# Optimization experiments

Measured on AMD Instinct MI355X. Metric: run time of the kernel, lower is better.

Reference implementation:

```python
import jax, jax.numpy as jnp
import numpy as np

N = 20000      # nodes
E = 640000     # edges (before self loops)
IN = 256       # in_channels == out_channels (forced by classifier size 4*in)
H1, C1 = 8, 16   # conv1: heads=8, out=16 -> concat 128
H2, C2 = 1, 256  # conv2: heads=1, out=out_channels
B = 4096       # article pairs
NEG_SLOPE = 0.2  # PyG GATv2Conv default negative_slope


def setup_inputs() -> dict:
    key = jax.random.key(0)
    ks = jax.random.split(key, 24)
    s = 0.05
    inp = {
        "gnn_x": jax.random.normal(ks[0], (N, IN), jnp.float32),
        "vanilla_x": jax.random.normal(ks[1], (N, IN), jnp.float32),
        "edge_src": jax.random.randint(ks[2], (E,), 0, N, jnp.int32),
        "edge_dst": jax.random.randint(ks[3], (E,), 0, N, jnp.int32),
        "a1_idx": jax.random.randint(ks[4], (B,), 0, N, jnp.int64),
        "a2_idx": jax.random.randint(ks[5], (B,), 0, N, jnp.int64),
        # conv1 params (lin_l, lin_r, att, bias)
        "Wl1": jax.random.normal(ks[6], (IN, H1 * C1), jnp.float32) * s,
        "bl1": jnp.zeros((H1 * C1,), jnp.float32),
        "Wr1": jax.random.normal(ks[7], (IN, H1 * C1), jnp.float32) * s,
        "br1": jnp.zeros((H1 * C1,), jnp.float32),
        "att1": jax.random.normal(ks[8], (H1, C1), jnp.float32) * s,
        "bias1": jnp.zeros((H1 * C1,), jnp.float32),
        # conv2 params
        "Wl2": jax.random.normal(ks[9], (H1 * C1, H2 * C2), jnp.float32) * s,
        "bl2": jnp.zeros((H2 * C2,), jnp.float32),
        "Wr2": jax.random.normal(ks[10], (H1 * C1, H2 * C2), jnp.float32) * s,
        "br2": jnp.zeros((H2 * C2,), jnp.float32),
        "att2": jax.random.normal(ks[11], (H2, C2), jnp.float32) * s,
        "bias2": jnp.zeros((H2 * C2,), jnp.float32),
        # classifier
        "Wc": jax.random.normal(ks[12], (4 * IN, 1), jnp.float32) * s,
        "bc": jnp.zeros((1,), jnp.float32),
    }
    return inp


def _gatv2_layer(x, src, dst, Wl, bl, Wr, br, att, bias):
    """GATv2Conv: x_l = lin_l(x)[src], x_r = lin_r(x)[dst];
    e = att . leaky_relu(x_l + x_r); segment softmax over dst; scatter-add x_l*alpha."""
    n = x.shape[0]
    h, c = att.shape
    xl = (x @ Wl + bl).reshape(n, h, c)
    xr = (x @ Wr + br).reshape(n, h, c)
    # per-edge attention logits [E, H]
    e = jnp.einsum('ehc,hc->eh', jax.nn.leaky_relu(xl[src] + xr[dst], NEG_SLOPE), att)
    # segment softmax over destination nodes (self loops guarantee non-empty segments)
    emax = jax.ops.segment_max(e, dst, num_segments=n)
    ex = jnp.exp(e - emax[dst])
    denom = jax.ops.segment_sum(ex, dst, num_segments=n)
    alpha = ex / denom[dst]                      # [E, H]
    out = jax.ops.segment_sum(alpha[:, :, None] * xl[src], dst, num_segments=n)  # [N,H,C]
    return out.reshape(n, h * c) + bias          # concat=True (heads=1 identical)


def reference(gnn_x, vanilla_x, Wl1, bl1, Wr1, br1, att1, bias1,
              Wl2, bl2, Wr2, br2, att2, bias2, Wc, bc,
              edge_src, edge_dst, a1_idx, a2_idx):
    n = gnn_x.shape[0]
    loops = jnp.arange(n, dtype=edge_src.dtype)
    src = jnp.concatenate([edge_src, loops])     # PyG add_self_loops=True
    dst = jnp.concatenate([edge_dst, loops])
    x = _gatv2_layer(gnn_x, src, dst, Wl1, bl1, Wr1, br1, att1, bias1)
    x = jax.nn.relu(x)
    x = _gatv2_layer(x, src, dst, Wl2, bl2, Wr2, br2, att2, bias2)
    combined = jnp.concatenate(
        [vanilla_x[a1_idx], vanilla_x[a2_idx], x[a1_idx], x[a2_idx]], axis=1)  # [B, 4*IN]
    logits = combined @ Wc + bc                  # [B, 1]
    return logits
```

## Files before the change

kernel.cpp:

```cpp
#include <hip/hip_runtime.h>
#include <math.h>

#define N_NODES 20000
#define M_PAD   20032
#define E_EDGES 640000
#define ET (E_EDGES + N_NODES)
#define IN_CH 256
#define D1 128
#define D2 256
#define BPAIRS 4096
#define NEG 0.2f
#define LOG2E 1.4426950408889634f

#define HIST_BLOCKS  ((ET + 255) / 256)
#define MARK_BLOCKS  (2 * BPAIRS / 256)
#define WCONV_BLOCKS 512
#define XCONV_BLOCKS (M_PAD * IN_CH / 4 / 4 / 256)

#if __has_builtin(__builtin_amdgcn_exp2f)
#define EXP2F(x) __builtin_amdgcn_exp2f(x)
#else
#define EXP2F(x) exp2f(x)
#endif

typedef __bf16 bf16x8 __attribute__((ext_vector_type(8)));
typedef float  f32x4  __attribute__((ext_vector_type(4)));
typedef float  f32x2  __attribute__((ext_vector_type(2)));
typedef unsigned short u16x4 __attribute__((ext_vector_type(4)));

__device__ __forceinline__ unsigned short f2b(float f) {
    unsigned int u = __float_as_uint(f);
    unsigned int r = u + 0x7FFFu + ((u >> 16) & 1u);
    return (unsigned short)(r >> 16);
}
__device__ __forceinline__ f32x2 up2(unsigned int u) {
    f32x2 r;
    r.x = __uint_as_float(u << 16);
    r.y = __uint_as_float(u & 0xFFFF0000u);
    return r;
}
__device__ __forceinline__ f32x2 lrelu2(f32x2 s) {
    return __builtin_elementwise_max(s, s * NEG);
}
__device__ __forceinline__ float lrelu(float s) { return fmaxf(s, NEG * s); }

__device__ __forceinline__ void unpack8(uint4 u, float* v) {
    v[0] = __uint_as_float(u.x << 16); v[1] = __uint_as_float(u.x & 0xFFFF0000u);
    v[2] = __uint_as_float(u.y << 16); v[3] = __uint_as_float(u.y & 0xFFFF0000u);
    v[4] = __uint_as_float(u.z << 16); v[5] = __uint_as_float(u.z & 0xFFFF0000u);
    v[6] = __uint_as_float(u.w << 16); v[7] = __uint_as_float(u.w & 0xFFFF0000u);
}


__global__ void prep_kernel(
        const float* __restrict__ gnn_x,
        const float* __restrict__ Wl1, const float* __restrict__ Wr1,
        const float* __restrict__ Wl2, const float* __restrict__ Wr2,
        const int* __restrict__ edge_dst,
        const int* __restrict__ a1_raw, const int* __restrict__ a2_raw,
        unsigned short* __restrict__ xb,
        unsigned short* __restrict__ wt1l, unsigned short* __restrict__ wt1r,
        unsigned short* __restrict__ wt2l, unsigned short* __restrict__ wt2r,
        int* __restrict__ count, int* __restrict__ rank,
        int* __restrict__ mark) {
    int bid = blockIdx.x;
    if (bid < HIST_BLOCKS) {
        int e = bid * 256 + threadIdx.x;
        if (e >= ET) return;
        int dst = (e < E_EDGES) ? edge_dst[e] : (e - E_EDGES);
        rank[e] = atomicAdd(&count[dst], 1);
    } else if (bid < HIST_BLOCKS + MARK_BLOCKS) {
        int idx = (bid - HIST_BLOCKS) * 256 + threadIdx.x;
        __shared__ int stride_s;
        if (threadIdx.x == 0) {
            bool i64 = true;
            for (int i = 1; i < 63; i += 2) i64 = i64 && (a1_raw[i] == 0);
            stride_s = i64 ? 2 : 1;
        }
        __syncthreads();
        int stride = stride_s;
        if (idx < BPAIRS) mark[a1_raw[(long)idx * stride]] = 1;
        else mark[a2_raw[(long)(idx - BPAIRS) * stride]] = 1;
    } else if (bid < HIST_BLOCKS + MARK_BLOCKS + WCONV_BLOCKS) {
        int idx = (bid - HIST_BLOCKS - MARK_BLOCKS) * 256 + threadIdx.x;
        int seg = idx >> 15;
        int r = idx & 32767;
        const float* W;
        unsigned short* Wt;
        int k, n, K;
        if (seg < 2) {
            W = seg ? Wr1 : Wl1; Wt = seg ? wt1r : wt1l;
            k = r >> 7; n = r & 127; K = IN_CH;
        } else {
            W = (seg & 1) ? Wr2 : Wl2; Wt = (seg & 1) ? wt2r : wt2l;
            k = r >> 8; n = r & 255; K = D1;
        }
        Wt[n * K + k] = f2b(W[r]);
    } else {
        int tid = (bid - HIST_BLOCKS - MARK_BLOCKS - WCONV_BLOCKS) * 256
                + threadIdx.x;
        const int NQ = M_PAD * IN_CH / 4;
        int q0 = tid * 4;
#pragma unroll
        for (int j = 0; j < 4; j++) {
            int qi = q0 + j;
            if (qi >= NQ) break;
            int e0 = qi * 4;
            int row = e0 >> 8;
            u16x4 o;
            if (row < N_NODES) {
                f32x4 v = __builtin_nontemporal_load((const f32x4*)(gnn_x + e0));
                o.x = f2b(v.x); o.y = f2b(v.y); o.z = f2b(v.z); o.w = f2b(v.w);
            } else {
                o.x = o.y = o.z = o.w = 0;
            }
            __builtin_nontemporal_store(o, (u16x4*)(xb + e0));
        }
    }
}


__global__ __launch_bounds__(1024) void scan_kernel(const int* __restrict__ count,
                                                    int* __restrict__ offsets) {
    const int PER = 20;
    int t = threadIdx.x;
    int base = t * PER;
    int local[PER];
    int sum = 0;
#pragma unroll
    for (int i = 0; i < PER; i++) {
        int idx = base + i;
        int v = (idx < N_NODES) ? count[idx] : 0;
        local[i] = sum;
        sum += v;
    }
    int lane = t & 63, wave = t >> 6;
    int s = sum;
#pragma unroll
    for (int off = 1; off < 64; off <<= 1) {
        int x = __shfl_up(s, off);
        if (lane >= off) s += x;
    }
    __shared__ int wsum[16];
    __shared__ int wpre[16];
    if (lane == 63) wsum[wave] = s;
    __syncthreads();
    if (t == 0) {
        int acc = 0;
        for (int w = 0; w < 16; w++) { wpre[w] = acc; acc += wsum[w]; }
        offsets[N_NODES] = acc;
    }
    __syncthreads();
    int thread_excl = wpre[wave] + (s - sum);
#pragma unroll
    for (int i = 0; i < PER; i++) {
        int idx = base + i;
        if (idx < N_NODES) offsets[idx] = thread_excl + local[i];
    }
}

__global__ void scatter_kernel(const int* __restrict__ edge_src,
                               const int* __restrict__ edge_dst,
                               const int* __restrict__ rank,
                               const int* __restrict__ offsets,
                               int* __restrict__ sorted_src) {
    int e = blockIdx.x * blockDim.x + threadIdx.x;
    if (e >= ET) return;
    int dst = (e < E_EDGES) ? edge_dst[e] : (e - E_EDGES);
    int src = (e < E_EDGES) ? edge_src[e] : (e - E_EDGES);
    sorted_src[offsets[dst] + rank[e]] = src;
}


template <int K>
__global__ __launch_bounds__(256) void dual_gemm_mfma_kernel(
        const unsigned short* __restrict__ A,
        const unsigned short* __restrict__ Wtl,
        const unsigned short* __restrict__ Wtr,
        const float* __restrict__ bl, const float* __restrict__ br,
        unsigned short* __restrict__ Yl, unsigned short* __restrict__ Yr,
        int M, int NOUT) {
    const int NK = K / 32;
    int wave = threadIdx.x >> 6;
    int lane = threadIdx.x & 63;
    int row0 = blockIdx.x * 64;
    int col0 = (blockIdx.y * 4 + wave) * 16;
    int rsub = lane & 15;
    int koff = (lane >> 4) * 8;

    const unsigned short* ap  = A   + (size_t)(row0 + rsub) * K + koff;
    const unsigned short* bpl = Wtl + (size_t)(col0 + rsub) * K + koff;
    const unsigned short* bpr = Wtr + (size_t)(col0 + rsub) * K + koff;

    bf16x8 bfl[NK], bfr[NK];
#pragma unroll
    for (int kb = 0; kb < NK; kb++) {
        bfl[kb] = *(const bf16x8*)(bpl + kb * 32);
        bfr[kb] = *(const bf16x8*)(bpr + kb * 32);
    }

    f32x4 l0 = {0.f, 0.f, 0.f, 0.f};
    f32x4 l1 = l0, l2 = l0, l3 = l0, r0 = l0, r1 = l0, r2 = l0, r3 = l0;

#pragma unroll
    for (int kb = 0; kb < NK; kb++) {
        int off = kb * 32;
        bf16x8 a0 = *(const bf16x8*)(ap + off);
        bf16x8 a1 = *(const bf16x8*)(ap + 16 * K + off);
        bf16x8 a2 = *(const bf16x8*)(ap + 32 * K + off);
        bf16x8 a3 = *(const bf16x8*)(ap + 48 * K + off);
        l0 = __builtin_amdgcn_mfma_f32_16x16x32_bf16(a0, bfl[kb], l0, 0, 0, 0);
        r0 = __builtin_amdgcn_mfma_f32_16x16x32_bf16(a0, bfr[kb], r0, 0, 0, 0);
        l1 = __builtin_amdgcn_mfma_f32_16x16x32_bf16(a1, bfl[kb], l1, 0, 0, 0);
        r1 = __builtin_amdgcn_mfma_f32_16x16x32_bf16(a1, bfr[kb], r1, 0, 0, 0);
        l2 = __builtin_amdgcn_mfma_f32_16x16x32_bf16(a2, bfl[kb], l2, 0, 0, 0);
        r2 = __builtin_amdgcn_mfma_f32_16x16x32_bf16(a2, bfr[kb], r2, 0, 0, 0);
        l3 = __builtin_amdgcn_mfma_f32_16x16x32_bf16(a3, bfl[kb], l3, 0, 0, 0);
        r3 = __builtin_amdgcn_mfma_f32_16x16x32_bf16(a3, bfr[kb], r3, 0, 0, 0);
    }

    int colg = col0 + rsub;
    float bvl = bl[colg];
    float bvr = br[colg];
    int rbase = row0 + (lane >> 4) * 4;
#pragma unroll
    for (int t = 0; t < 4; t++) {
        f32x4 al = (t == 0) ? l0 : (t == 1) ? l1 : (t == 2) ? l2 : l3;
        f32x4 ar = (t == 0) ? r0 : (t == 1) ? r1 : (t == 2) ? r2 : r3;
#pragma unroll
        for (int r = 0; r < 4; r++) {
            int row = rbase + t * 16 + r;
            if (row < M) {
                Yl[(size_t)row * NOUT + colg] = f2b(al[r] + bvl);
                Yr[(size_t)row * NOUT + colg] = f2b(ar[r] + bvr);
            }
        }
    }
}


__global__ __launch_bounds__(256) void aggregate1_kernel(
        const unsigned short* __restrict__ xl1, const unsigned short* __restrict__ xr1,
        const float* __restrict__ att1, const float* __restrict__ bias1,
        const int* __restrict__ offsets, const int* __restrict__ sorted_src,
        unsigned short* __restrict__ x1) {
    int wave = threadIdx.x >> 6;
    int lane = threadIdx.x & 63;
    int q = lane >> 4;
    int ql = lane & 15;
    int dst = blockIdx.x * 4 + wave;
    if (dst >= M_PAD) return;
    int c0 = ql * 8;
    if (dst >= N_NODES) {
        if (q == 0) {
            uint4 z; z.x = z.y = z.z = z.w = 0;
            *(uint4*)(x1 + (size_t)dst * D1 + c0) = z;
        }
        return;
    }

    uint4 xu = *(const uint4*)(xr1 + (size_t)dst * D1 + c0);
    f32x2 xr[4] = {up2(xu.x), up2(xu.y), up2(xu.z), up2(xu.w)};
    float4 aa0 = *(const float4*)(att1 + c0);
    float4 aa1 = *(const float4*)(att1 + c0 + 4);
    f32x2 att[4];
    att[0].x = aa0.x * LOG2E; att[0].y = aa0.y * LOG2E;
    att[1].x = aa0.z * LOG2E; att[1].y = aa0.w * LOG2E;
    att[2].x = aa1.x * LOG2E; att[2].y = aa1.y * LOG2E;
    att[3].x = aa1.z * LOG2E; att[3].y = aa1.w * LOG2E;

    int beg = offsets[dst], end = offsets[dst + 1];
    const unsigned short* base = xl1 + c0;

    float l = 0.f;
    f32x2 acc[4] = {{0.f,0.f},{0.f,0.f},{0.f,0.f},{0.f,0.f}};

    int i = beg;
    int s0 = sorted_src[min(i + q, end - 1)];
    uint4 g0 = *(const uint4*)(base + (size_t)s0 * D1);
    while (true) {
        int inext = i + 4;
        bool more = inext < end;
        uint4 g1;
        if (more) {
            int s1 = sorted_src[min(inext + q, end - 1)];
            g1 = *(const uint4*)(base + (size_t)s1 * D1);
        }
        bool act = (i + q) < end;
        f32x2 v0 = up2(g0.x), v1 = up2(g0.y), v2 = up2(g0.z), v3 = up2(g0.w);
        f32x2 p2 = att[0] * lrelu2(v0 + xr[0]);
        p2 += att[1] * lrelu2(v1 + xr[1]);
        p2 += att[2] * lrelu2(v2 + xr[2]);
        p2 += att[3] * lrelu2(v3 + xr[3]);
        float p = p2.x + p2.y;
        p += __shfl_xor(p, 1);
        float w = act ? EXP2F(p) : 0.f;
        l += w;
        acc[0] += w * v0; acc[1] += w * v1; acc[2] += w * v2; acc[3] += w * v3;
        if (!more) break;
        i = inext; g0 = g1;
    }
    l += __shfl_xor(l, 16);
    l += __shfl_xor(l, 32);
#pragma unroll
    for (int j = 0; j < 4; j++) {
        f32x2 t;
        t.x = __shfl_xor(acc[j].x, 16); t.y = __shfl_xor(acc[j].y, 16);
        acc[j] += t;
        t.x = __shfl_xor(acc[j].x, 32); t.y = __shfl_xor(acc[j].y, 32);
        acc[j] += t;
    }
    if (q == 0) {
        float inv = 1.f / l;
        float4 bb0 = *(const float4*)(bias1 + c0);
        float4 bb1 = *(const float4*)(bias1 + c0 + 4);
        unsigned short o[8];
        o[0] = f2b(fmaxf(acc[0].x * inv + bb0.x, 0.f));
        o[1] = f2b(fmaxf(acc[0].y * inv + bb0.y, 0.f));
        o[2] = f2b(fmaxf(acc[1].x * inv + bb0.z, 0.f));
        o[3] = f2b(fmaxf(acc[1].y * inv + bb0.w, 0.f));
        o[4] = f2b(fmaxf(acc[2].x * inv + bb1.x, 0.f));
        o[5] = f2b(fmaxf(acc[2].y * inv + bb1.y, 0.f));
        o[6] = f2b(fmaxf(acc[3].x * inv + bb1.z, 0.f));
        o[7] = f2b(fmaxf(acc[3].y * inv + bb1.w, 0.f));
        uint4 ov;
        ov.x = (unsigned int)o[0] | ((unsigned int)o[1] << 16);
        ov.y = (unsigned int)o[2] | ((unsigned int)o[3] << 16);
        ov.z = (unsigned int)o[4] | ((unsigned int)o[5] << 16);
        ov.w = (unsigned int)o[6] | ((unsigned int)o[7] << 16);
        *(uint4*)(x1 + (size_t)dst * D1 + c0) = ov;
    }
}


__global__ __launch_bounds__(256) void aggregate2_kernel(
        const unsigned short* __restrict__ xl2, const unsigned short* __restrict__ xr2,
        const float* __restrict__ att2, const float* __restrict__ bias2,
        const int* __restrict__ offsets, const int* __restrict__ sorted_src,
        const int* __restrict__ mark,
        float* __restrict__ x2) {
    int wave = threadIdx.x >> 6;
    int lane = threadIdx.x & 63;
    int half = lane >> 5;
    int hl = lane & 31;
    int dst = blockIdx.x * 4 + wave;
    if (dst >= N_NODES) return;
    if (!mark[dst]) return;
    int c0 = hl * 8;

    float xr[8], att[8];
    unpack8(*(const uint4*)(xr2 + (size_t)dst * D2 + c0), xr);
#pragma unroll
    for (int j = 0; j < 8; j++) att[j] = att2[c0 + j] * LOG2E;
    int beg = offsets[dst], end = offsets[dst + 1];

    float l = 0.f;
    float acc[8];
#pragma unroll
    for (int j = 0; j < 8; j++) acc[j] = 0.f;

    int i = beg;
    for (; i + 4 <= end; i += 4) {
        int sA = sorted_src[i + half];
        int sB = sorted_src[i + 2 + half];
        float vA[8], vB[8];
        unpack8(*(const uint4*)(xl2 + (size_t)sA * D2 + c0), vA);
        unpack8(*(const uint4*)(xl2 + (size_t)sB * D2 + c0), vB);
        float pA = 0.f, pB = 0.f;
#pragma unroll
        for (int j = 0; j < 8; j++) pA = fmaf(att[j], lrelu(vA[j] + xr[j]), pA);
#pragma unroll
        for (int j = 0; j < 8; j++) pB = fmaf(att[j], lrelu(vB[j] + xr[j]), pB);
        pA += __shfl_xor(pA, 1);  pB += __shfl_xor(pB, 1);
        pA += __shfl_xor(pA, 2);  pB += __shfl_xor(pB, 2);
        pA += __shfl_xor(pA, 4);  pB += __shfl_xor(pB, 4);
        pA += __shfl_xor(pA, 8);  pB += __shfl_xor(pB, 8);
        pA += __shfl_xor(pA, 16); pB += __shfl_xor(pB, 16);
        float wA = EXP2F(pA), wB = EXP2F(pB);
        l += wA + wB;
#pragma unroll
        for (int j = 0; j < 8; j++) acc[j] += wA * vA[j] + wB * vB[j];
    }
    for (; i + 2 <= end; i += 2) {
        int sA = sorted_src[i + half];
        float vA[8];
        unpack8(*(const uint4*)(xl2 + (size_t)sA * D2 + c0), vA);
        float pA = 0.f;
#pragma unroll
        for (int j = 0; j < 8; j++) pA = fmaf(att[j], lrelu(vA[j] + xr[j]), pA);
        pA += __shfl_xor(pA, 1);
        pA += __shfl_xor(pA, 2);
        pA += __shfl_xor(pA, 4);
        pA += __shfl_xor(pA, 8);
        pA += __shfl_xor(pA, 16);
        float wA = EXP2F(pA);
        l += wA;
#pragma unroll
        for (int j = 0; j < 8; j++) acc[j] += wA * vA[j];
    }
    if (i < end && half == 0) {
        int sA = sorted_src[i];
        float vA[8];
        unpack8(*(const uint4*)(xl2 + (size_t)sA * D2 + c0), vA);
        float pA = 0.f;
#pragma unroll
        for (int j = 0; j < 8; j++) pA = fmaf(att[j], lrelu(vA[j] + xr[j]), pA);
        pA += __shfl_xor(pA, 1);
        pA += __shfl_xor(pA, 2);
        pA += __shfl_xor(pA, 4);
        pA += __shfl_xor(pA, 8);
        pA += __shfl_xor(pA, 16);
        float wA = EXP2F(pA);
        l += wA;
#pragma unroll
        for (int j = 0; j < 8; j++) acc[j] += wA * vA[j];
    }
    l += __shfl_xor(l, 32);
#pragma unroll
    for (int j = 0; j < 8; j++) acc[j] += __shfl_xor(acc[j], 32);
    if (half == 0) {
        float inv = 1.f / l;
        float4 o0, o1;
        o0.x = acc[0] * inv + bias2[c0 + 0];
        o0.y = acc[1] * inv + bias2[c0 + 1];
        o0.z = acc[2] * inv + bias2[c0 + 2];
        o0.w = acc[3] * inv + bias2[c0 + 3];
        o1.x = acc[4] * inv + bias2[c0 + 4];
        o1.y = acc[5] * inv + bias2[c0 + 5];
        o1.z = acc[6] * inv + bias2[c0 + 6];
        o1.w = acc[7] * inv + bias2[c0 + 7];
        *(float4*)(x2 + (size_t)dst * D2 + c0) = o0;
        *(float4*)(x2 + (size_t)dst * D2 + c0 + 4) = o1;
    }
}


__global__ __launch_bounds__(256) void classifier_kernel(
        const float* __restrict__ vanilla_x, const float* __restrict__ x2,
        const int* __restrict__ a1_raw, const int* __restrict__ a2_raw,
        const float* __restrict__ Wc, const float* __restrict__ bc,
        float* __restrict__ out) {
    int b = blockIdx.x;
    int t = threadIdx.x;

    __shared__ int stride_s;
    if (t == 0) {
        bool i64 = true;
        for (int i = 1; i < 63; i += 2) i64 = i64 && (a1_raw[i] == 0);
        stride_s = i64 ? 2 : 1;
    }
    __syncthreads();
    int stride = stride_s;
    int a1 = a1_raw[(long)b * stride];
    int a2 = a2_raw[(long)b * stride];

    float s = vanilla_x[a1 * IN_CH + t] * Wc[t]
            + vanilla_x[a2 * IN_CH + t] * Wc[IN_CH + t]
            + x2[a1 * D2 + t] * Wc[2 * IN_CH + t]
            + x2[a2 * D2 + t] * Wc[3 * IN_CH + t];
    s += __shfl_xor(s, 1);
    s += __shfl_xor(s, 2);
    s += __shfl_xor(s, 4);
    s += __shfl_xor(s, 8);
    s += __shfl_xor(s, 16);
    s += __shfl_xor(s, 32);
    __shared__ float part[4];
    if ((t & 63) == 0) part[t >> 6] = s;
    __syncthreads();
    if (t == 0) out[b] = part[0] + part[1] + part[2] + part[3] + bc[0];
}


extern "C" void kernel_launch(void* const* d_in, const int* in_sizes, int n_in,
                              void* d_out, int out_size, void* d_ws, size_t ws_size,
                              hipStream_t stream) {
    const float* gnn_x     = (const float*)d_in[0];
    const float* vanilla_x = (const float*)d_in[1];
    const int*   edge_src  = (const int*)d_in[2];
    const int*   edge_dst  = (const int*)d_in[3];
    const int*   a1_idx    = (const int*)d_in[4];
    const int*   a2_idx    = (const int*)d_in[5];
    const float* Wl1   = (const float*)d_in[6];
    const float* bl1   = (const float*)d_in[7];
    const float* Wr1   = (const float*)d_in[8];
    const float* br1   = (const float*)d_in[9];
    const float* att1  = (const float*)d_in[10];
    const float* bias1 = (const float*)d_in[11];
    const float* Wl2   = (const float*)d_in[12];
    const float* bl2   = (const float*)d_in[13];
    const float* Wr2   = (const float*)d_in[14];
    const float* br2   = (const float*)d_in[15];
    const float* att2  = (const float*)d_in[16];
    const float* bias2 = (const float*)d_in[17];
    const float* Wc    = (const float*)d_in[18];
    const float* bc    = (const float*)d_in[19];
    float* out = (float*)d_out;

    char* p = (char*)d_ws;
    unsigned short* xb   = (unsigned short*)p; p += (size_t)M_PAD * IN_CH * 2;
    unsigned short* x1b  = (unsigned short*)p; p += (size_t)M_PAD * D1 * 2;
    unsigned short* xl1b = (unsigned short*)p; p += (size_t)N_NODES * D1 * 2;
    unsigned short* xr1b = (unsigned short*)p; p += (size_t)N_NODES * D1 * 2;
    unsigned short* xl2b = (unsigned short*)p; p += (size_t)N_NODES * D2 * 2;
    unsigned short* xr2b = (unsigned short*)p; p += (size_t)N_NODES * D2 * 2;
    unsigned short* wt1l = (unsigned short*)p; p += (size_t)D1 * IN_CH * 2;
    unsigned short* wt1r = (unsigned short*)p; p += (size_t)D1 * IN_CH * 2;
    unsigned short* wt2l = (unsigned short*)p; p += (size_t)D2 * D1 * 2;
    unsigned short* wt2r = (unsigned short*)p; p += (size_t)D2 * D1 * 2;
    float* x2 = (float*)p; p += (size_t)N_NODES * D2 * 4;
    int* count      = (int*)p; p += (size_t)N_NODES * 4;
    int* mark       = (int*)p; p += (size_t)N_NODES * 4;
    int* offsets    = (int*)p; p += (size_t)(N_NODES + 4) * 4;
    int* rank       = (int*)p; p += (size_t)ET * 4;
    int* sorted_src = (int*)p; p += (size_t)ET * 4;

    hipMemsetAsync(count, 0, (size_t)2 * N_NODES * sizeof(int), stream);

    prep_kernel<<<HIST_BLOCKS + MARK_BLOCKS + WCONV_BLOCKS + XCONV_BLOCKS,
                  256, 0, stream>>>(
        gnn_x, Wl1, Wr1, Wl2, Wr2, edge_dst, a1_idx, a2_idx,
        xb, wt1l, wt1r, wt2l, wt2r, count, rank, mark);
    scan_kernel<<<1, 1024, 0, stream>>>(count, offsets);
    scatter_kernel<<<HIST_BLOCKS, 256, 0, stream>>>(
        edge_src, edge_dst, rank, offsets, sorted_src);

    dim3 g1(M_PAD / 64, D1 / 64);
    dual_gemm_mfma_kernel<IN_CH><<<g1, 256, 0, stream>>>(
        xb, wt1l, wt1r, bl1, br1, xl1b, xr1b, N_NODES, D1);
    aggregate1_kernel<<<M_PAD / 4, 256, 0, stream>>>(
        xl1b, xr1b, att1, bias1, offsets, sorted_src, x1b);

    dim3 g2(M_PAD / 64, D2 / 64);
    dual_gemm_mfma_kernel<D1><<<g2, 256, 0, stream>>>(
        x1b, wt2l, wt2r, bl2, br2, xl2b, xr2b, N_NODES, D2);
    aggregate2_kernel<<<(N_NODES + 3) / 4, 256, 0, stream>>>(
        xl2b, xr2b, att2, bias2, offsets, sorted_src, mark, x2);

    classifier_kernel<<<BPAIRS, 256, 0, stream>>>(
        vanilla_x, x2, a1_idx, a2_idx, Wc, bc, out);
}
```

Baseline: 291.3 us.

## Replace global-atomic degree histogram with per-block LDS histograms and prefix

The CSR build used one global atomicAdd per edge to count in-degree and assign ranks. It now has 128 blocks, each building a shared-memory histogram over its own edge chunk in two halves of the node range. A new kernel prefix-sums these per-block counts across blocks to get per-node totals, and the scatter adds the block's offset to each edge's rank. This avoids contended global atomics but adds a 128×N count buffer (aliased onto xl2b), an extra launch, and two passes over the edges per block. The xb store also changes from nontemporal to a normal store.

```diff
diff --git a/kernel.cpp b/kernel.cpp
--- a/kernel.cpp
+++ b/kernel.cpp
@@ -12,7 +12,10 @@
 #define NEG 0.2f
 #define LOG2E 1.4426950408889634f
 
-#define HIST_BLOCKS  ((ET + 255) / 256)
+#define NB_HIST   128
+#define CHUNK     ((ET + NB_HIST - 1) / NB_HIST)
+#define HALF_BINS 10000
+
 #define MARK_BLOCKS  (2 * BPAIRS / 256)
 #define WCONV_BLOCKS 512
 #define XCONV_BLOCKS (M_PAD * IN_CH / 4 / 4 / 256)
@@ -52,7 +55,7 @@
 }
 
 
-__global__ void prep_kernel(
+__global__ __launch_bounds__(256) void prep_kernel(
         const float* __restrict__ gnn_x,
         const float* __restrict__ Wl1, const float* __restrict__ Wr1,
         const float* __restrict__ Wl2, const float* __restrict__ Wr2,
@@ -61,16 +64,31 @@
         unsigned short* __restrict__ xb,
         unsigned short* __restrict__ wt1l, unsigned short* __restrict__ wt1r,
         unsigned short* __restrict__ wt2l, unsigned short* __restrict__ wt2r,
-        int* __restrict__ count, int* __restrict__ rank,
+        int* __restrict__ cb,
+        int* __restrict__ rank,
         int* __restrict__ mark) {
+    __shared__ int lc[HALF_BINS];
     int bid = blockIdx.x;
-    if (bid < HIST_BLOCKS) {
-        int e = bid * 256 + threadIdx.x;
-        if (e >= ET) return;
-        int dst = (e < E_EDGES) ? edge_dst[e] : (e - E_EDGES);
-        rank[e] = atomicAdd(&count[dst], 1);
-    } else if (bid < HIST_BLOCKS + MARK_BLOCKS) {
-        int idx = (bid - HIST_BLOCKS) * 256 + threadIdx.x;
+    if (bid < NB_HIST) {
+        int ebeg = bid * CHUNK;
+        int eend = min(ebeg + CHUNK, ET);
+#pragma unroll 1
+        for (int half = 0; half < 2; half++) {
+            int lo = half * HALF_BINS;
+            for (int i = threadIdx.x; i < HALF_BINS; i += 256) lc[i] = 0;
+            __syncthreads();
+            for (int e = ebeg + threadIdx.x; e < eend; e += 256) {
+                int dst = (e < E_EDGES) ? edge_dst[e] : (e - E_EDGES);
+                int d = dst - lo;
+                if (0 <= d && d < HALF_BINS) rank[e] = atomicAdd(&lc[d], 1);
+            }
+            __syncthreads();
+            for (int i = threadIdx.x; i < HALF_BINS; i += 256)
+                cb[(size_t)bid * N_NODES + lo + i] = lc[i];
+            __syncthreads();
+        }
+    } else if (bid < NB_HIST + MARK_BLOCKS) {
+        int idx = (bid - NB_HIST) * 256 + threadIdx.x;
         __shared__ int stride_s;
         if (threadIdx.x == 0) {
             bool i64 = true;
@@ -81,8 +99,8 @@
         int stride = stride_s;
         if (idx < BPAIRS) mark[a1_raw[(long)idx * stride]] = 1;
         else mark[a2_raw[(long)(idx - BPAIRS) * stride]] = 1;
-    } else if (bid < HIST_BLOCKS + MARK_BLOCKS + WCONV_BLOCKS) {
-        int idx = (bid - HIST_BLOCKS - MARK_BLOCKS) * 256 + threadIdx.x;
+    } else if (bid < NB_HIST + MARK_BLOCKS + WCONV_BLOCKS) {
+        int idx = (bid - NB_HIST - MARK_BLOCKS) * 256 + threadIdx.x;
         int seg = idx >> 15;
         int r = idx & 32767;
         const float* W;
@@ -97,7 +115,7 @@
         }
         Wt[n * K + k] = f2b(W[r]);
     } else {
-        int tid = (bid - HIST_BLOCKS - MARK_BLOCKS - WCONV_BLOCKS) * 256
+        int tid = (bid - NB_HIST - MARK_BLOCKS - WCONV_BLOCKS) * 256
                 + threadIdx.x;
         const int NQ = M_PAD * IN_CH / 4;
         int q0 = tid * 4;
@@ -114,9 +132,25 @@
             } else {
                 o.x = o.y = o.z = o.w = 0;
             }
-            __builtin_nontemporal_store(o, (u16x4*)(xb + e0));
-        }
-    }
+            *(u16x4*)(xb + e0) = o;
+        }
+    }
+}
+
+
+__global__ __launch_bounds__(256) void repprefix_kernel(
+        int* __restrict__ cb, int* __restrict__ count) {
+    int dst = blockIdx.x * 256 + threadIdx.x;
+    if (dst >= N_NODES) return;
+    int run = 0;
+#pragma unroll 4
+    for (int r = 0; r < NB_HIST; r++) {
+        size_t idx = (size_t)r * N_NODES + dst;
+        int c = cb[idx];
+        cb[idx] = run;
+        run += c;
+    }
+    count[dst] = run;
 }
 
 
@@ -163,12 +197,14 @@
                                const int* __restrict__ edge_dst,
                                const int* __restrict__ rank,
                                const int* __restrict__ offsets,
+                               const int* __restrict__ cb,
                                int* __restrict__ sorted_src) {
     int e = blockIdx.x * blockDim.x + threadIdx.x;
     if (e >= ET) return;
     int dst = (e < E_EDGES) ? edge_dst[e] : (e - E_EDGES);
     int src = (e < E_EDGES) ? edge_src[e] : (e - E_EDGES);
-    sorted_src[offsets[dst] + rank[e]] = src;
+    int rep = e / CHUNK;
+    sorted_src[offsets[dst] + cb[(size_t)rep * N_NODES + dst] + rank[e]] = src;
 }
 
 
@@ -513,16 +549,18 @@
     int* offsets    = (int*)p; p += (size_t)(N_NODES + 4) * 4;
     int* rank       = (int*)p; p += (size_t)ET * 4;
     int* sorted_src = (int*)p; p += (size_t)ET * 4;
-
-    hipMemsetAsync(count, 0, (size_t)2 * N_NODES * sizeof(int), stream);
-
-    prep_kernel<<<HIST_BLOCKS + MARK_BLOCKS + WCONV_BLOCKS + XCONV_BLOCKS,
+    int* cb = (int*)xl2b;
+
+    hipMemsetAsync(mark, 0, (size_t)N_NODES * sizeof(int), stream);
+
+    prep_kernel<<<NB_HIST + MARK_BLOCKS + WCONV_BLOCKS + XCONV_BLOCKS,
                   256, 0, stream>>>(
         gnn_x, Wl1, Wr1, Wl2, Wr2, edge_dst, a1_idx, a2_idx,
-        xb, wt1l, wt1r, wt2l, wt2r, count, rank, mark);
+        xb, wt1l, wt1r, wt2l, wt2r, cb, rank, mark);
+    repprefix_kernel<<<(N_NODES + 255) / 256, 256, 0, stream>>>(cb, count);
     scan_kernel<<<1, 1024, 0, stream>>>(count, offsets);
-    scatter_kernel<<<HIST_BLOCKS, 256, 0, stream>>>(
-        edge_src, edge_dst, rank, offsets, sorted_src);
+    scatter_kernel<<<(ET + 255) / 256, 256, 0, stream>>>(
+        edge_src, edge_dst, rank, offsets, cb, sorted_src);
 
     dim3 g1(M_PAD / 64, D1 / 64);
     dual_gemm_mfma_kernel<IN_CH><<<g1, 256, 0, stream>>>(
```

Result: faster. 283.1 us (-2.8%).
